# Performance work log

Hardware: AMD Instinct MI355X
Metric: run time of the kernel (lower is better)

The kernel has to match this reference:

```python
import jax, jax.numpy as jnp
import numpy as np

V, E, SH, H = 30000, 1024, 2048, 1024   # vocab, emb_size, ses_hid_size, hid_size
B, T = 64, 50
PAD = 10003
H2 = 2 * H  # GRU hidden size


def setup_inputs() -> dict:
    key = jax.random.key(0)
    ks = jax.random.split(key, 12)
    s = 0.02
    emb_W = jax.random.normal(ks[2], (V, E), jnp.float32) * s
    emb_W = emb_W.at[PAD].set(0.0)  # padding_idx row is zero
    return {
        "ses_encoding": jax.random.normal(ks[0], (B, 1, SH), jnp.float32),
        "x": jax.random.randint(ks[1], (B, T), 0, V),
        "emb_W": emb_W,
        "gru_Wih": jax.random.normal(ks[3], (3 * H2, E), jnp.float32) * s,
        "gru_Whh": jax.random.normal(ks[4], (3 * H2, H2), jnp.float32) * s,
        "gru_bih": jax.random.normal(ks[5], (3 * H2,), jnp.float32) * s,
        "gru_bhh": jax.random.normal(ks[6], (3 * H2,), jnp.float32) * s,
        "lin1_W": jax.random.normal(ks[7], (H, SH), jnp.float32) * s,
        "lin1_b": jax.random.normal(ks[8], (H,), jnp.float32) * s,
        "lin2_W": jax.random.normal(ks[9], (E, H2), jnp.float32) * s,
        "lin2_b": jax.random.normal(ks[10], (E,), jnp.float32) * s,
        "out_W": jax.random.normal(ks[11], (V, E), jnp.float32) * s,
    }


def reference(ses_encoding, x, emb_W, gru_Wih, gru_Whh, gru_bih, gru_bhh,
              lin1_W, lin1_b, lin2_W, lin2_b, out_W):
    # ses_encoding: [B,1,SH] -> tanh(lin1) -> [B,1,H] -> view [1,B,H] -> [B,H]
    ses = jnp.tanh(jnp.einsum('bos,hs->boh', ses_encoding, lin1_W) + lin1_b)
    ses_enc = ses.reshape(B, H)  # [B, H]

    toks = x.T  # [T, B], teacher-forced inputs
    tok_next = jnp.concatenate([x[:, 1:], jnp.zeros((B, 1), x.dtype)], axis=1).T  # [T, B]
    has_next = jnp.arange(T) < (T - 1)  # [T]

    def step(h, xs):
        tok, nxt, hn = xs  # tok: [B]
        emb = jnp.where((tok == PAD)[:, None], 0.0, emb_W[tok])  # [B, E] (dropout=eval identity)
        hcat = jnp.concatenate([h, ses_enc], axis=-1)  # [B, 2H]
        gi = emb @ gru_Wih.T + gru_bih    # [B, 6H]
        gh = hcat @ gru_Whh.T + gru_bhh   # [B, 6H]
        i_r, i_z, i_n = jnp.split(gi, 3, axis=-1)
        h_r, h_z, h_n = jnp.split(gh, 3, axis=-1)
        r = jax.nn.sigmoid(i_r + h_r)
        z = jax.nn.sigmoid(i_z + h_z)
        n = jnp.tanh(i_n + r * h_n)
        h_full = (1.0 - z) * n + z * hcat     # [B, 2H]
        h_next = h_full[:, :H]                # keep first hid_size half
        hid_o = h_full @ lin2_W.T + lin2_b + emb  # [B, E]
        logits = hid_o @ out_W.T              # [B, V]
        logp = jax.nn.log_softmax(logits, axis=-1)
        ll = jnp.where(hn, logp[jnp.arange(B), nxt], 0.0)  # [B]
        return h_next, (logits, ll)

    _, (all_logits, all_ll) = jax.lax.scan(step, ses_enc, (toks, tok_next, has_next))
    dec_o = jnp.transpose(all_logits, (1, 0, 2))  # [B, T, V]
    log_l = jnp.sum(all_ll, axis=0)               # [B]
    return dec_o, log_l
```

## Files before the change

### kernel.cpp

```cpp
#include <hip/hip_runtime.h>
#include <hip/hip_bf16.h>
#include <stdint.h>

#define VV   30000
#define EE   1024
#define SHH  2048
#define HH   1024
#define H2   2048
#define G3   6144
#define BB   64
#define TT   50
#define PADT 10003
#define MM   3200
#define NPAD 30080
#define RBLK 64
#define PNB  (NPAD / 64)

typedef __bf16 bf16;
typedef bf16  bf16x8 __attribute__((ext_vector_type(8)));
typedef bf16  bf16x4v __attribute__((ext_vector_type(4)));
typedef float f32x4 __attribute__((ext_vector_type(4)));

__device__ __forceinline__ void async16(void* lds_base, const void* gsrc) {
    __builtin_amdgcn_global_load_lds(
        (const __attribute__((address_space(1))) void*)gsrc,
        (__attribute__((address_space(3))) void*)lds_base, 16, 0, 0);
}

__device__ __forceinline__ int xcd_swizzle(int lin, int nwg) {
    int q = nwg >> 3, r = nwg & 7;
    int x = lin & 7, o = lin >> 3;
    return (x < r ? x * (q + 1) : r * (q + 1) + (x - r) * q) + o;
}

__device__ __forceinline__ float sigmoidf_(float x) {
    return 1.f / (1.f + __expf(-x));
}

__global__ __launch_bounds__(256) void k_conv(bf16* dst, const float* src, int n) {
    int i = (blockIdx.x * 256 + threadIdx.x) * 4;
    if (i + 3 >= n) return;
    float4 v = *(const float4*)&src[i];
    bf16x4v o; o[0] = (bf16)v.x; o[1] = (bf16)v.y; o[2] = (bf16)v.z; o[3] = (bf16)v.w;
    *(bf16x4v*)&dst[i] = o;
}

__global__ __launch_bounds__(256) void k_conv_outw(bf16* dst, const float* src) {
    int row = blockIdx.x;
    int c = threadIdx.x * 4;
    bf16x4v o;
    if (row < VV) {
        float4 v = *(const float4*)&src[(size_t)row * EE + c];
        o[0] = (bf16)v.x; o[1] = (bf16)v.y; o[2] = (bf16)v.z; o[3] = (bf16)v.w;
    } else {
        o[0] = (bf16)0.f; o[1] = (bf16)0.f; o[2] = (bf16)0.f; o[3] = (bf16)0.f;
    }
    *(bf16x4v*)&dst[(size_t)row * EE + c] = o;
}

__global__ __launch_bounds__(256) void k_conv_whhhi(bf16* dst, const float* whh) {
    int d = blockIdx.x;
    int cblk = d / 192, rem = d % 192, g = rem / 64, s = rem % 64;
    const float* srow = whh + (size_t)(g * H2 + 1024 + cblk * 64 + s) * H2;
    int c = threadIdx.x * 4;
    float4 v = *(const float4*)&srow[c];
    bf16x4v o; o[0] = (bf16)v.x; o[1] = (bf16)v.y; o[2] = (bf16)v.z; o[3] = (bf16)v.w;
    *(bf16x4v*)&dst[(size_t)d * HH + c] = o;
}

__global__ __launch_bounds__(256) void k_embed(const int* x, const float* embW, bf16* out) {
    int i = blockIdx.x;
    int t = i >> 6, b = i & 63;
    int tok = x[b * TT + t];
    int e = threadIdx.x * 4;
    bf16x4v o;
    if (tok == PADT) {
        o[0] = (bf16)0.f; o[1] = (bf16)0.f; o[2] = (bf16)0.f; o[3] = (bf16)0.f;
    } else {
        float4 v = *(const float4*)&embW[(size_t)tok * EE + e];
        o[0] = (bf16)v.x; o[1] = (bf16)v.y; o[2] = (bf16)v.z; o[3] = (bf16)v.w;
    }
    *(bf16x4v*)&out[(size_t)i * EE + e] = o;
}

template<int KIND>
__global__ __launch_bounds__(256)
void sgemm64(const float* __restrict__ A, const float* __restrict__ Bm,
             const float* __restrict__ bias, float* __restrict__ Of, bf16* __restrict__ Ob,
             int N, int K, int lda, int ldb, int koff, int ldo) {
    int n0 = blockIdx.x * 64;
    int tid = threadIdx.x;
    int tr = tid >> 4, tc = tid & 15;
    __shared__ float As[64][33];
    __shared__ float Bs[64][33];
    float acc[4][4] = {};
    for (int k0 = 0; k0 < K; k0 += 32) {
        #pragma unroll
        for (int q = 0; q < 8; ++q) {
            int p = q * 256 + tid; int r = p >> 5, kk = p & 31;
            As[r][kk] = A[(size_t)r * lda + k0 + kk];
            Bs[r][kk] = Bm[(size_t)(n0 + r) * ldb + koff + k0 + kk];
        }
        __syncthreads();
        #pragma unroll
        for (int kk = 0; kk < 32; ++kk) {
            float a4[4], b4[4];
            #pragma unroll
            for (int i = 0; i < 4; i++) a4[i] = As[tr * 4 + i][kk];
            #pragma unroll
            for (int j = 0; j < 4; j++) b4[j] = Bs[tc * 4 + j][kk];
            #pragma unroll
            for (int i = 0; i < 4; i++)
                #pragma unroll
                for (int j = 0; j < 4; j++) acc[i][j] += a4[i] * b4[j];
        }
        __syncthreads();
    }
    #pragma unroll
    for (int i = 0; i < 4; i++)
        #pragma unroll
        for (int j = 0; j < 4; j++) {
            int row = tr * 4 + i, col = n0 + tc * 4 + j;
            float v = acc[i][j] + bias[col];
            if (KIND == 0) {
                v = tanhf(v);
                Of[(size_t)row * N + col] = v;
                Ob[(size_t)row * ldo + col] = (bf16)v;
            } else {
                Of[(size_t)row * N + col] = v;
            }
        }
}

template<int KIND>
__global__ __launch_bounds__(256)
void gemm128(const bf16* __restrict__ A, const bf16* __restrict__ Bm,
             void* __restrict__ Cout, const float* __restrict__ bias,
             const bf16* __restrict__ addend, float* __restrict__ pm,
             float* __restrict__ ps, int N, int K, int lda, int ldb, int Nreal) {
    int nwg = gridDim.x * gridDim.y;
    int lin = blockIdx.y * gridDim.x + blockIdx.x;
    int wg = xcd_swizzle(lin, nwg);
    int bx = wg % gridDim.x, by = wg / gridDim.x;
    const int n0 = bx * 128;
    const int m0 = by * 128;
    const int tid = threadIdx.x;
    const int w = tid >> 6, l = tid & 63;
    const int wr = w >> 1, wc = w & 1;
    __shared__ bf16 As[128 * 32];
    __shared__ bf16 Bs[128 * 32];
    f32x4 acc[4][4] = {};
    const int lrow = l >> 2;
    const int lk = (l & 3) * 8;
    for (int kt = 0; kt < K; kt += 32) {
        #pragma unroll
        for (int q = 0; q < 2; ++q) {
            int ch = w * 2 + q;
            async16(&As[ch * 512], A + (size_t)(m0 + ch * 16 + lrow) * lda + kt + lk);
            async16(&Bs[ch * 512], Bm + (size_t)(n0 + ch * 16 + lrow) * ldb + kt + lk);
        }
        __syncthreads();
        bf16x8 af[4], bfr[4];
        #pragma unroll
        for (int mi = 0; mi < 4; mi++)
            af[mi] = *(const bf16x8*)&As[(wr * 64 + mi * 16 + (l & 15)) * 32 + (l >> 4) * 8];
        #pragma unroll
        for (int ni = 0; ni < 4; ni++)
            bfr[ni] = *(const bf16x8*)&Bs[(wc * 64 + ni * 16 + (l & 15)) * 32 + (l >> 4) * 8];
        #pragma unroll
        for (int mi = 0; mi < 4; mi++)
            #pragma unroll
            for (int ni = 0; ni < 4; ni++)
                acc[mi][ni] = __builtin_amdgcn_mfma_f32_16x16x32_bf16(af[mi], bfr[ni], acc[mi][ni], 0, 0, 0);
        __syncthreads();
    }
    #pragma unroll
    for (int mi = 0; mi < 4; mi++)
        #pragma unroll
        for (int ni = 0; ni < 4; ni++) {
            int row0 = m0 + wr * 64 + mi * 16 + (l >> 4) * 4;
            int col = n0 + wc * 64 + ni * 16 + (l & 15);
            f32x4 v = acc[mi][ni];
            #pragma unroll
            for (int r = 0; r < 4; r++) {
                int rr = row0 + r;
                float xv = v[r];
                if constexpr (KIND == 0 || KIND == 1) xv += bias[col];
                if constexpr (KIND == 1) xv += (float)addend[(size_t)rr * N + col];
                if constexpr (KIND == 2) {
                    if (col < Nreal) {
                        int t = rr >> 6, b = rr & 63;
                        ((float*)Cout)[((size_t)(b * TT + t)) * VV + col] = xv;
                    }
                } else {
                    ((bf16*)Cout)[(size_t)rr * N + col] = (bf16)xv;
                }
            }
        }
    if constexpr (KIND == 2) {
        #pragma unroll
        for (int mi = 0; mi < 4; mi++) {
            #pragma unroll
            for (int r = 0; r < 4; r++) {
                float m = -1e30f, s = 0.f;
                #pragma unroll
                for (int ni = 0; ni < 4; ni++) {
                    int col = n0 + wc * 64 + ni * 16 + (l & 15);
                    if (col < Nreal) {
                        float v = acc[mi][ni][r];
                        float M = fmaxf(m, v);
                        s = s * __expf(m - M) + __expf(v - M);
                        m = M;
                    }
                }
                #pragma unroll
                for (int off = 1; off < 16; off <<= 1) {
                    float m2 = __shfl_xor(m, off);
                    float s2 = __shfl_xor(s, off);
                    float M = fmaxf(m, m2);
                    s = s * __expf(m - M) + s2 * __expf(m2 - M);
                    m = M;
                }
                if ((l & 15) == 0) {
                    int row = m0 + wr * 64 + mi * 16 + (l >> 4) * 4 + r;
                    size_t pidx = (size_t)row * PNB + (n0 >> 6) + wc;
                    pm[pidx] = m; ps[pidx] = s;
                }
            }
        }
    }
}

__global__ __launch_bounds__(384, 1)
void k_rnn(const float* __restrict__ Whh,
           const bf16* __restrict__ gi_b,
           const float* __restrict__ ghs,
           bf16* __restrict__ hfx,
           uint32_t* __restrict__ ctr) {
    const int blk = blockIdx.x;
    const int c0 = blk * 16;
    const int tid = threadIdx.x;
    const int wv = tid >> 6;
    const int l  = tid & 63;
    const int g  = wv >> 1;
    const int mh = wv & 1;
    const int lc = l & 15, lk = l >> 4;
    __shared__ char h_lds[131072];
    __shared__ float ghl[3][64][17];

    bf16x8 breg[32];
    {
        const float* wrow = Whh + ((size_t)(g * H2 + c0 + lc)) * H2;
        #pragma unroll
        for (int kt = 0; kt < 32; ++kt) {
            const float* p = wrow + kt * 32 + lk * 8;
            float4 v0 = *(const float4*)p;
            float4 v1 = *(const float4*)(p + 4);
            bf16x8 o;
            o[0] = (bf16)v0.x; o[1] = (bf16)v0.y; o[2] = (bf16)v0.z; o[3] = (bf16)v0.w;
            o[4] = (bf16)v1.x; o[5] = (bf16)v1.y; o[6] = (bf16)v1.z; o[7] = (bf16)v1.w;
            breg[kt] = o;
        }
    }
    float pr[4], pz[4], pn[4];
    if (wv < 4) {
        #pragma unroll
        for (int r = 0; r < 4; ++r) {
            int b = wv * 16 + lk * 4 + r;
            size_t base = (size_t)b * G3 + c0 + lc;
            pr[r] = ghs[base];
            pz[r] = ghs[base + H2];
            pn[r] = ghs[base + 2 * H2];
        }
    }

    for (int t = 0; t < TT; ++t) {
        bf16 qr[4], qz[4], qn[4];
        if (wv < 4) {
            const bf16* gp = gi_b + ((size_t)t * BB) * G3;
            #pragma unroll
            for (int r = 0; r < 4; ++r) {
                int b = wv * 16 + lk * 4 + r;
                size_t base = (size_t)b * G3 + c0 + lc;
                qr[r] = gp[base];
                qz[r] = gp[base + H2];
                qn[r] = gp[base + 2 * H2];
            }
        }

        {
            const uint64_t* hsrc = (const uint64_t*)(hfx + (size_t)t * BB * H2);
            #pragma unroll 1
            for (int i0 = 0; i0 < 48; i0 += 16) {
                uint64_t v[16];
                #pragma unroll
                for (int j = 0; j < 16; ++j) {
                    int idx = (i0 + j) * 384 + tid;
                    v[j] = (idx < 16384)
                        ? __hip_atomic_load(hsrc + idx, __ATOMIC_RELAXED, __HIP_MEMORY_SCOPE_AGENT)
                        : 0ull;
                }
                #pragma unroll
                for (int j = 0; j < 16; ++j) {
                    int idx = (i0 + j) * 384 + tid;
                    if (idx < 16384) {
                        int byte = idx * 8;
                        int swb = byte ^ (((byte >> 11) & 7) << 4);
                        *(uint64_t*)(h_lds + swb) = v[j];
                    }
                }
            }
        }
        __syncthreads();

        f32x4 acc0 = {}, acc1 = {};
        const int r0 = mh * 32 + lc, r1 = r0 + 16;
        const int sw = (lc & 7) << 4;
        #pragma unroll
        for (int kt = 0; kt < 32; ++kt) {
            int cbyte = kt * 64 + lk * 16;
            bf16x8 a0 = *(const bf16x8*)(h_lds + ((r0 * 2048 + cbyte) ^ sw));
            bf16x8 a1 = *(const bf16x8*)(h_lds + ((r1 * 2048 + cbyte) ^ sw));
            acc0 = __builtin_amdgcn_mfma_f32_16x16x32_bf16(a0, breg[kt], acc0, 0, 0, 0);
            acc1 = __builtin_amdgcn_mfma_f32_16x16x32_bf16(a1, breg[kt], acc1, 0, 0, 0);
        }
        #pragma unroll
        for (int r = 0; r < 4; ++r) {
            ghl[g][mh * 32 + lk * 4 + r][lc]      = acc0[r];
            ghl[g][mh * 32 + 16 + lk * 4 + r][lc] = acc1[r];
        }
        __syncthreads();

        if (wv < 4) {
            #pragma unroll
            for (int r = 0; r < 4; ++r) {
                int b = wv * 16 + lk * 4 + r;
                float hr = ghl[0][b][lc] + pr[r];
                float hz = ghl[1][b][lc] + pz[r];
                float hn = ghl[2][b][lc] + pn[r];
                float rg = sigmoidf_((float)qr[r] + hr);
                float zg = sigmoidf_((float)qz[r] + hz);
                float ng = tanhf((float)qn[r] + rg * hn);
                int hvb = (b * 2048 + (c0 + lc) * 2) ^ ((b & 7) << 4);
                float hv = (float)*(const bf16*)(h_lds + hvb);
                float hf = (1.f - zg) * ng + zg * hv;
                union { bf16 h; uint16_t u; } cv;
                cv.h = (bf16)hf;
                __hip_atomic_store(
                    (uint16_t*)&hfx[((size_t)(t + 1) * BB + b) * H2 + c0 + lc],
                    cv.u, __ATOMIC_RELAXED, __HIP_MEMORY_SCOPE_AGENT);
            }
        }

        if (t != TT - 1) {
            __syncthreads();
            if (tid == 0) {
                __hip_atomic_fetch_add(&ctr[t], 1u, __ATOMIC_RELAXED, __HIP_MEMORY_SCOPE_AGENT);
                while (__hip_atomic_load(&ctr[t], __ATOMIC_RELAXED, __HIP_MEMORY_SCOPE_AGENT) < RBLK)
                    __builtin_amdgcn_s_sleep(1);
            }
            __syncthreads();
        }
    }
}

__global__ __launch_bounds__(256)
void k_hi(const bf16* __restrict__ hfx_,
          const float* __restrict__ ses_f,
          const bf16* __restrict__ Wrh,
          const bf16* __restrict__ gi_b,
          const float* __restrict__ ghs,
          bf16* __restrict__ hfx_out) {
    const int cblk = blockIdx.x;
    const int t    = blockIdx.y;
    const int tid = threadIdx.x;
    const int w = tid >> 6, l = tid & 63;
    __shared__ bf16 As[64 * 32];
    __shared__ bf16 Bs[192 * 32];
    f32x4 acc[12] = {};
    const int lrow = l >> 2;
    const int lk = (l & 3) * 8;
    const bf16* Abase = hfx_ + ((size_t)t * BB) * H2;
    for (int kt = 0; kt < HH; kt += 32) {
        async16(&As[w * 512], Abase + (size_t)(w * 16 + lrow) * H2 + kt + lk);
        #pragma unroll
        for (int q = 0; q < 3; ++q) {
            int cb = w * 3 + q;
            async16(&Bs[cb * 512], Wrh + (size_t)(cblk * 192 + cb * 16 + lrow) * HH + kt + lk);
        }
        __syncthreads();
        bf16x8 af = *(const bf16x8*)&As[(w * 16 + (l & 15)) * 32 + (l >> 4) * 8];
        #pragma unroll
        for (int j = 0; j < 12; j++) {
            bf16x8 bfj = *(const bf16x8*)&Bs[(j * 16 + (l & 15)) * 32 + (l >> 4) * 8];
            acc[j] = __builtin_amdgcn_mfma_f32_16x16x32_bf16(af, bfj, acc[j], 0, 0, 0);
        }
        __syncthreads();
    }
    #pragma unroll
    for (int jc = 0; jc < 4; jc++) {
        int ch = cblk * 64 + jc * 16 + (l & 15);
        #pragma unroll
        for (int r = 0; r < 4; r++) {
            int b = w * 16 + (l >> 4) * 4 + r;
            size_t gb = (size_t)(t * BB + b) * G3 + 1024 + ch;
            size_t sb = (size_t)b * G3 + 1024 + ch;
            float gr = (float)gi_b[gb];
            float gz = (float)gi_b[gb + H2];
            float gn = (float)gi_b[gb + 2 * H2];
            float hr = acc[jc][r]     + ghs[sb];
            float hz = acc[4 + jc][r] + ghs[sb + H2];
            float hn = acc[8 + jc][r] + ghs[sb + 2 * H2];
            float rg = sigmoidf_(gr + hr);
            float zg = sigmoidf_(gz + hz);
            float ng = tanhf(gn + rg * hn);
            float hv = ses_f[b * HH + ch];
            float hf = (1.f - zg) * ng + zg * hv;
            hfx_out[((size_t)(t + 1) * BB + b) * H2 + HH + ch] = (bf16)hf;
        }
    }
}

__global__ void k_lse(const float* __restrict__ pm, const float* __restrict__ ps,
                      const float* __restrict__ logits, const int* __restrict__ x,
                      float* __restrict__ ll) {
    int row = blockIdx.x;
    int t = row >> 6, b = row & 63;
    int l = threadIdx.x;
    float m = -1e30f, s = 0.f;
    for (int i = l; i < PNB; i += 64) {
        float mi = pm[(size_t)row * PNB + i];
        float si = ps[(size_t)row * PNB + i];
        float M = fmaxf(m, mi);
        s = s * __expf(m - M) + si * __expf(mi - M);
        m = M;
    }
    #pragma unroll
    for (int off = 32; off; off >>= 1) {
        float m2 = __shfl_down(m, off);
        float s2 = __shfl_down(s, off);
        float M = fmaxf(m, m2);
        s = s * __expf(m - M) + s2 * __expf(m2 - M);
        m = M;
    }
    if (l == 0) {
        float v = 0.f;
        if (t < TT - 1) {
            int nxt = x[b * TT + t + 1];
            v = logits[((size_t)(b * TT + t)) * VV + nxt] - (m + __logf(s));
        }
        ll[row] = v;
    }
}

__global__ void k_sumll(const float* __restrict__ ll_ws, float* __restrict__ out) {
    int b = threadIdx.x;
    if (b < BB) {
        float s = 0.f;
        for (int t = 0; t < TT; t++) s += ll_ws[t * BB + b];
        out[b] = s;
    }
}

extern "C" void kernel_launch(void* const* d_in, const int* in_sizes, int n_in,
                              void* d_out, int out_size, void* d_ws, size_t ws_size,
                              hipStream_t stream) {
    const float* ses_encoding = (const float*)d_in[0];
    const int*   x            = (const int*)d_in[1];
    const float* emb_W        = (const float*)d_in[2];
    const float* gru_Wih      = (const float*)d_in[3];
    const float* gru_Whh      = (const float*)d_in[4];
    const float* gru_bih      = (const float*)d_in[5];
    const float* gru_bhh      = (const float*)d_in[6];
    const float* lin1_W       = (const float*)d_in[7];
    const float* lin1_b       = (const float*)d_in[8];
    const float* lin2_W       = (const float*)d_in[9];
    const float* lin2_b       = (const float*)d_in[10];
    const float* out_W        = (const float*)d_in[11];

    char* W = (char*)d_ws;
    size_t off = 0;
    auto take = [&](size_t bytes) { void* p = W + off; off += (bytes + 255) & ~(size_t)255; return p; };

    float* ses_f32 = (float*)take((size_t)BB * HH * 4);
    bf16* Wih_b    = (bf16*)take((size_t)G3 * EE * 2);
    bf16* Wrh_b    = (bf16*)take((size_t)3072 * HH * 2);
    bf16* lin2_b16 = (bf16*)take((size_t)EE * H2 * 2);
    bf16* outW_b   = (bf16*)take((size_t)NPAD * EE * 2);
    bf16* emb_b    = (bf16*)take((size_t)MM * EE * 2);
    bf16* gi_b     = (bf16*)take((size_t)MM * G3 * 2);
    float* ghs     = (float*)take((size_t)BB * G3 * 4);
    bf16* hfx      = (bf16*)take((size_t)(TT + 1) * BB * H2 * 2);
    bf16* hido_b   = (bf16*)take((size_t)MM * EE * 2);
    float* ll_ws   = (float*)take((size_t)MM * 4);
    float* pm      = (float*)take((size_t)MM * PNB * 4);
    float* ps      = (float*)take((size_t)MM * PNB * 4);
    uint32_t* ctr  = (uint32_t*)take((size_t)TT * 4);

    hipMemsetAsync(ctr, 0, TT * 4, stream);

    k_conv<<<(G3 * EE) / 1024, 256, 0, stream>>>(Wih_b, gru_Wih, G3 * EE);
    k_conv<<<(EE * H2) / 1024, 256, 0, stream>>>(lin2_b16, lin2_W, EE * H2);
    k_conv_outw<<<NPAD, 256, 0, stream>>>(outW_b, out_W);
    k_conv_whhhi<<<3072, 256, 0, stream>>>(Wrh_b, gru_Whh);
    k_embed<<<MM, 256, 0, stream>>>(x, emb_W, emb_b);

    sgemm64<0><<<HH / 64, 256, 0, stream>>>(ses_encoding, lin1_W, lin1_b, ses_f32, hfx,
                                            HH, SHH, SHH, SHH, 0, H2);
    sgemm64<1><<<G3 / 64, 256, 0, stream>>>(ses_f32, gru_Whh, gru_bhh, ghs, nullptr,
                                            G3, HH, HH, H2, HH, 0);

    gemm128<0><<<dim3(G3 / 128, MM / 128), 256, 0, stream>>>(
        emb_b, Wih_b, gi_b, gru_bih, nullptr, nullptr, nullptr, G3, EE, EE, EE, 0);

    k_rnn<<<RBLK, 384, 0, stream>>>(gru_Whh, gi_b, ghs, hfx, ctr);

    k_hi<<<dim3(16, TT), 256, 0, stream>>>(hfx, ses_f32, Wrh_b, gi_b, ghs, hfx);

    gemm128<1><<<dim3(EE / 128, MM / 128), 256, 0, stream>>>(
        hfx + (size_t)BB * H2, lin2_b16, hido_b, lin2_b, emb_b, nullptr, nullptr,
        EE, H2, H2, H2, 0);

    gemm128<2><<<dim3(NPAD / 128, MM / 128), 256, 0, stream>>>(
        hido_b, outW_b, d_out, nullptr, nullptr, pm, ps, NPAD, EE, EE, EE, VV);

    k_lse<<<MM, 64, 0, stream>>>(pm, ps, (const float*)d_out, x, ll_ws);
    k_sumll<<<1, 64, 0, stream>>>(ll_ws, (float*)d_out + (size_t)BB * TT * VV);
}
```

Before: 1.540 ms.

## Use hierarchical grid barrier, nontemporal logits stores, and wider h prefetch batches

Replaces the flat per-step atomic counter barrier in the persistent GRU kernel with a two-level tree: groups of 8 blocks increment padded group counters, the last arrival of each group bumps a root counter, and the final arrival sets a flag that every block polls. The barrier now also uses release/acquire ordering. This is meant to cut contention on a single atomic and the latency of the 49 per-step grid syncs. The logits GEMM epilogue also writes its large fp32 output with nontemporal stores to avoid cache pollution, and the hidden-state load loop issues 22 loads per batch instead of 16, which raises register pressure.

```diff
diff --git a/kernel.cpp b/kernel.cpp
--- a/kernel.cpp
+++ b/kernel.cpp
@@ -190,7 +190,8 @@
                 if constexpr (KIND == 2) {
                     if (col < Nreal) {
                         int t = rr >> 6, b = rr & 63;
-                        ((float*)Cout)[((size_t)(b * TT + t)) * VV + col] = xv;
+                        __builtin_nontemporal_store(
+                            xv, &((float*)Cout)[((size_t)(b * TT + t)) * VV + col]);
                     }
                 } else {
                     ((bf16*)Cout)[(size_t)rr * N + col] = (bf16)xv;
@@ -236,7 +237,9 @@
            const bf16* __restrict__ gi_b,
            const float* __restrict__ ghs,
            bf16* __restrict__ hfx,
-           uint32_t* __restrict__ ctr) {
+           uint32_t* __restrict__ ctrg,
+           uint32_t* __restrict__ root,
+           uint32_t* __restrict__ flag) {
     const int blk = blockIdx.x;
     const int c0 = blk * 16;
     const int tid = threadIdx.x;
@@ -291,17 +294,17 @@
         {
             const uint64_t* hsrc = (const uint64_t*)(hfx + (size_t)t * BB * H2);
             #pragma unroll 1
-            for (int i0 = 0; i0 < 48; i0 += 16) {
-                uint64_t v[16];
+            for (int i0 = 0; i0 < 44; i0 += 22) {
+                uint64_t v[22];
                 #pragma unroll
-                for (int j = 0; j < 16; ++j) {
+                for (int j = 0; j < 22; ++j) {
                     int idx = (i0 + j) * 384 + tid;
                     v[j] = (idx < 16384)
                         ? __hip_atomic_load(hsrc + idx, __ATOMIC_RELAXED, __HIP_MEMORY_SCOPE_AGENT)
                         : 0ull;
                 }
                 #pragma unroll
-                for (int j = 0; j < 16; ++j) {
+                for (int j = 0; j < 22; ++j) {
                     int idx = (i0 + j) * 384 + tid;
                     if (idx < 16384) {
                         int byte = idx * 8;
@@ -355,9 +358,18 @@
         if (t != TT - 1) {
             __syncthreads();
             if (tid == 0) {
-                __hip_atomic_fetch_add(&ctr[t], 1u, __ATOMIC_RELAXED, __HIP_MEMORY_SCOPE_AGENT);
-                while (__hip_atomic_load(&ctr[t], __ATOMIC_RELAXED, __HIP_MEMORY_SCOPE_AGENT) < RBLK)
-                    __builtin_amdgcn_s_sleep(1);
+                uint32_t* cg = ctrg + ((size_t)t * 8 + (blk >> 3)) * 32;
+                if (__hip_atomic_fetch_add(cg, 1u, __ATOMIC_RELEASE, __HIP_MEMORY_SCOPE_AGENT) == 7u) {
+                    uint32_t* rt = root + (size_t)t * 32;
+                    if (__hip_atomic_fetch_add(rt, 1u, __ATOMIC_RELEASE, __HIP_MEMORY_SCOPE_AGENT) == 7u) {
+                        __hip_atomic_store(flag + (size_t)t * 32, 1u,
+                                           __ATOMIC_RELEASE, __HIP_MEMORY_SCOPE_AGENT);
+                    }
+                }
+                while (__hip_atomic_load(flag + (size_t)t * 32,
+                                         __ATOMIC_RELAXED, __HIP_MEMORY_SCOPE_AGENT) == 0u)
+                    __builtin_amdgcn_s_sleep(2);
+                __builtin_amdgcn_fence(__ATOMIC_ACQUIRE, "agent");
             }
             __syncthreads();
         }
@@ -495,9 +507,13 @@
     float* ll_ws   = (float*)take((size_t)MM * 4);
     float* pm      = (float*)take((size_t)MM * PNB * 4);
     float* ps      = (float*)take((size_t)MM * PNB * 4);
-    uint32_t* ctr  = (uint32_t*)take((size_t)TT * 4);
-
-    hipMemsetAsync(ctr, 0, TT * 4, stream);
+    uint32_t* ctrg = (uint32_t*)take((size_t)TT * 8 * 32 * 4);
+    uint32_t* root = (uint32_t*)take((size_t)TT * 32 * 4);
+    uint32_t* flag = (uint32_t*)take((size_t)TT * 32 * 4);
+
+    hipMemsetAsync(ctrg, 0, (size_t)TT * 8 * 32 * 4, stream);
+    hipMemsetAsync(root, 0, (size_t)TT * 32 * 4, stream);
+    hipMemsetAsync(flag, 0, (size_t)TT * 32 * 4, stream);
 
     k_conv<<<(G3 * EE) / 1024, 256, 0, stream>>>(Wih_b, gru_Wih, G3 * EE);
     k_conv<<<(EE * H2) / 1024, 256, 0, stream>>>(lin2_b16, lin2_W, EE * H2);
@@ -513,7 +529,7 @@
     gemm128<0><<<dim3(G3 / 128, MM / 128), 256, 0, stream>>>(
         emb_b, Wih_b, gi_b, gru_bih, nullptr, nullptr, nullptr, G3, EE, EE, EE, 0);
 
-    k_rnn<<<RBLK, 384, 0, stream>>>(gru_Whh, gi_b, ghs, hfx, ctr);
+    k_rnn<<<RBLK, 384, 0, stream>>>(gru_Whh, gi_b, ghs, hfx, ctrg, root, flag);
 
     k_hi<<<dim3(16, TT), 256, 0, stream>>>(hfx, ses_f32, Wrh_b, gi_b, ghs, hfx);
 
```

New measurement: 1.531 ms. About the same (-0.6%).
